# Performance work log

Measured on AMD Instinct MI355X. Metric: run time of the kernel, lower is better.

Reference implementation:

```python
import jax, jax.numpy as jnp
import numpy as np

D_K = 64
NEG_INF = -1.0e9

def setup_inputs() -> dict:
    key = jax.random.key(0)
    kq, kk, kv, km = jax.random.split(key, 4)
    B, H, S, D = 2, 16, 2048, D_K
    Q = jax.random.normal(kq, (B, H, S, D), dtype=jnp.float32)
    K = jax.random.normal(kk, (B, H, S, D), dtype=jnp.float32)
    V = jax.random.normal(kv, (B, H, S, D), dtype=jnp.float32)
    # True entries are masked out (torch masked_fill semantics)
    attn_mask = jax.random.randint(km, (B, H, S, S), 0, 2).astype(jnp.bool_)
    return {"Q": Q, "K": K, "V": V, "attn_mask": attn_mask}

def reference(Q, K, V, attn_mask):
    # scores: [B, H, len_q, len_k]
    scale = 1.0 / np.sqrt(D_K).astype(np.float32)
    scores = jnp.einsum('bhqd,bhkd->bhqk', Q, K) * scale
    scores = jnp.where(attn_mask, jnp.float32(NEG_INF), scores)
    attn = jax.nn.softmax(scores, axis=-1)
    prob = jnp.einsum('bhqk,bhkd->bhqd', attn, V)
    return (prob, attn)
```

## Files before the change

kernel.cpp:

```cpp
#include <hip/hip_runtime.h>
#include <hip/hip_bf16.h>

#define S_LEN 2048
#define D_DIM 64
#define QT    64
#define KT    64
#define NTHR  256
#define NKT   (S_LEN / KT)
#define NBLK  1024
#define PROB_ELEMS 4194304LL

typedef float        f32x4  __attribute__((ext_vector_type(4)));
typedef int          i32x4  __attribute__((ext_vector_type(4)));
typedef unsigned int u32x4  __attribute__((ext_vector_type(4)));
typedef short        bf16x8 __attribute__((ext_vector_type(8)));

__device__ __forceinline__ unsigned short f2bf(float f) {
    return __builtin_bit_cast(unsigned short, __float2bfloat16(f));
}
__device__ __forceinline__ int swzc(int row, int ch) {
    return ch ^ ((row ^ (row >> 3)) & 7);
}
__device__ __forceinline__ u32x4 packbf(float4 a, float4 b) {
    u32x4 r;
    r[0] = (unsigned)f2bf(a.x) | ((unsigned)f2bf(a.y) << 16);
    r[1] = (unsigned)f2bf(a.z) | ((unsigned)f2bf(a.w) << 16);
    r[2] = (unsigned)f2bf(b.x) | ((unsigned)f2bf(b.y) << 16);
    r[3] = (unsigned)f2bf(b.z) | ((unsigned)f2bf(b.w) << 16);
    return r;
}

__global__ void mask_probe_kernel(const unsigned int* __restrict__ m,
                                  int* __restrict__ flag) {
    unsigned int v = m[threadIdx.x];
    unsigned long long ok = __ballot(v <= 1u);
    if (threadIdx.x == 0) *flag = (ok == ~0ULL) ? 1 : 0;
}


#define LOAD_K(KP, KTV)                                                     \
    { _Pragma("unroll")                                                     \
      for (int i = 0; i < 2; ++i) {                                         \
        int flat = i * NTHR + t, row = flat >> 3, ch = flat & 7;            \
        const float* src = Kg + (kbase + (KTV) * KT + row) * D_DIM + ch * 8;\
        float4 a = *(const float4*)src, b = *(const float4*)(src + 4);      \
        KP[i] = packbf(a, b);                                               \
      } }

#define STAGE_K(KS, KP)                                                     \
    { _Pragma("unroll")                                                     \
      for (int i = 0; i < 2; ++i) {                                         \
        int flat = i * NTHR + t, row = flat >> 3, ch = flat & 7;            \
        *(u32x4*)((KS) + row * 128 + swzc(row, ch) * 16) = KP[i];           \
      } }

#define LOAD_V(VP, KTV)                                                     \
    { const float* src = Vg + (kbase + (KTV) * KT + k0v) * D_DIM + dgv * 8; \
      float4 a = *(const float4*)src, b = *(const float4*)(src + 4);        \
      float4 e4 = *(const float4*)(src + D_DIM);                            \
      float4 f4 = *(const float4*)(src + D_DIM + 4);                        \
      VP[0] = (unsigned)f2bf(a.x) | ((unsigned)f2bf(e4.x) << 16);           \
      VP[1] = (unsigned)f2bf(a.y) | ((unsigned)f2bf(e4.y) << 16);           \
      VP[2] = (unsigned)f2bf(a.z) | ((unsigned)f2bf(e4.z) << 16);           \
      VP[3] = (unsigned)f2bf(a.w) | ((unsigned)f2bf(e4.w) << 16);           \
      VP[4] = (unsigned)f2bf(b.x) | ((unsigned)f2bf(f4.x) << 16);           \
      VP[5] = (unsigned)f2bf(b.y) | ((unsigned)f2bf(f4.y) << 16);           \
      VP[6] = (unsigned)f2bf(b.z) | ((unsigned)f2bf(f4.z) << 16);           \
      VP[7] = (unsigned)f2bf(b.w) | ((unsigned)f2bf(f4.w) << 16); }

#define STAGE_V(VT, VP)                                                     \
    { _Pragma("unroll")                                                     \
      for (int jj = 0; jj < 8; ++jj) {                                      \
        int d = dgv * 8 + jj;                                               \
        *(unsigned*)((VT) + d * 128 + swzc(d, k0v >> 3) * 16 + (k0v & 7) * 2) = VP[jj]; \
      } }

#define LOAD_MBITS(DST, KTV)                                                \
    { unsigned bz = 0u;                                                     \
      _Pragma("unroll")                                                     \
      for (int n = 0; n < 4; ++n) {                                         \
        unsigned idx = rowoff + (unsigned)((KTV) * KT + n * 16 + 4 * g);    \
        if (mask32) {                                                       \
            i32x4 m4 = *(const i32x4*)(((const int*)maskB) + idx);          \
            bz |= ((m4[0] ? 1u : 0u) | (m4[1] ? 2u : 0u) |                  \
                   (m4[2] ? 4u : 0u) | (m4[3] ? 8u : 0u)) << (n * 4);       \
        } else {                                                            \
            unsigned mb = *(const unsigned*)(maskB + idx);                  \
            bz |= (((mb & 0xffu) ? 1u : 0u) | ((mb & 0xff00u) ? 2u : 0u) |  \
                   ((mb & 0xff0000u) ? 4u : 0u) |                           \
                   ((mb & 0xff000000u) ? 8u : 0u)) << (n * 4);              \
        } }                                                                 \
      (DST) = bz; }

#define LOAD_BITS2(DST, KTV)                                                \
    { if (useWS) (DST) = (unsigned)bitsWS[bitbase + (unsigned)(KTV) * NTHR];\
      else LOAD_MBITS(DST, KTV) }

#define PH1_TILE(KS, BITS)                                                  \
    { unsigned bb = (BITS);                                                 \
      _Pragma("unroll")                                                     \
      for (int n = 0; n < 4; ++n) {                                         \
        int rowk = n * 16 + c;                                              \
        bf16x8 kf0 = *(const bf16x8*)((KS) + rowk * 128 + swzc(rowk, g) * 16);     \
        bf16x8 kf1 = *(const bf16x8*)((KS) + rowk * 128 + swzc(rowk, 4 + g) * 16); \
        f32x4 acc = {0.f, 0.f, 0.f, 0.f};                                   \
        acc = __builtin_amdgcn_mfma_f32_16x16x32_bf16(kf0, qf0, acc, 0, 0, 0); \
        acc = __builtin_amdgcn_mfma_f32_16x16x32_bf16(kf1, qf1, acc, 0, 0, 0); \
        unsigned mb = bb >> (n * 4);                                        \
        psum += (mb & 1u) ? 0.f : __expf(acc[0] * 0.125f);                  \
        psum += (mb & 2u) ? 0.f : __expf(acc[1] * 0.125f);                  \
        psum += (mb & 4u) ? 0.f : __expf(acc[2] * 0.125f);                  \
        psum += (mb & 8u) ? 0.f : __expf(acc[3] * 0.125f);                  \
      } }

#define PH2_TILE(KS, VT, BITS, KTV)                                         \
    { unsigned bb = (BITS);                                                 \
      _Pragma("unroll")                                                     \
      for (int n = 0; n < 4; ++n) {                                         \
        int rowk = n * 16 + c;                                              \
        bf16x8 kf0 = *(const bf16x8*)((KS) + rowk * 128 + swzc(rowk, g) * 16);     \
        bf16x8 kf1 = *(const bf16x8*)((KS) + rowk * 128 + swzc(rowk, 4 + g) * 16); \
        f32x4 acc = {0.f, 0.f, 0.f, 0.f};                                   \
        acc = __builtin_amdgcn_mfma_f32_16x16x32_bf16(kf0, qf0, acc, 0, 0, 0); \
        acc = __builtin_amdgcn_mfma_f32_16x16x32_bf16(kf1, qf1, acc, 0, 0, 0); \
        unsigned mb = bb >> (n * 4);                                        \
        f32x4 ev;                                                           \
        ev[0] = (mb & 1u) ? 0.f : __expf(acc[0] * 0.125f) * rinv;           \
        ev[1] = (mb & 2u) ? 0.f : __expf(acc[1] * 0.125f) * rinv;           \
        ev[2] = (mb & 4u) ? 0.f : __expf(acc[2] * 0.125f) * rinv;           \
        ev[3] = (mb & 8u) ? 0.f : __expf(acc[3] * 0.125f) * rinv;           \
        unsigned idx0 = rowoff + (unsigned)((KTV) * KT + n * 16 + 4 * g);   \
        __builtin_nontemporal_store(ev, (f32x4*)(attnOut + idx0));          \
        unsigned p0 = (unsigned)f2bf(ev[0]) | ((unsigned)f2bf(ev[1]) << 16);\
        unsigned p1 = (unsigned)f2bf(ev[2]) | ((unsigned)f2bf(ev[3]) << 16);\
        int kloc = n * 16 + 4 * g;                                          \
        uint2 pkv; pkv.x = p0; pkv.y = p1;                                  \
        *(uint2*)(Ps + ql * 128 + swzc(ql, kloc >> 3) * 16 + (kloc & 7) * 2) = pkv; \
      }                                                                     \
             \
      { bf16x8 pa0 = *(const bf16x8*)(Ps + ql * 128 + swzc(ql, g) * 16);    \
        bf16x8 pa1 = *(const bf16x8*)(Ps + ql * 128 + swzc(ql, 4 + g) * 16);\
        _Pragma("unroll")                                                   \
        for (int df = 0; df < 4; ++df) {                                    \
            int d = df * 16 + c;                                            \
            bf16x8 vb0 = *(const bf16x8*)((VT) + d * 128 + swzc(d, g) * 16);     \
            bf16x8 vb1 = *(const bf16x8*)((VT) + d * 128 + swzc(d, 4 + g) * 16); \
            pacc[df] = __builtin_amdgcn_mfma_f32_16x16x32_bf16(pa0, vb0, pacc[df], 0, 0, 0); \
            pacc[df] = __builtin_amdgcn_mfma_f32_16x16x32_bf16(pa1, vb1, pacc[df], 0, 0, 0); \
        } } }

__global__ __launch_bounds__(NTHR, 4)
void attn_fused(const float* __restrict__ Qg, const float* __restrict__ Kg,
                const float* __restrict__ Vg,
                const unsigned char* __restrict__ maskB,
                const int* __restrict__ flagp,
                unsigned short* __restrict__ bitsWS, int useWS,
                float* __restrict__ attnOut, float* __restrict__ probOut) {
    __shared__ unsigned char sm[40960];
    unsigned char* Ks0 = sm;
    unsigned char* Ks1 = sm + 8192;
    unsigned char* Vt0 = sm + 16384;
    unsigned char* Vt1 = sm + 24576;
    unsigned char* Ps  = sm + 32768;

    const int t = threadIdx.x;
    const int lane = t & 63, w = t >> 6, c = lane & 15, g = lane >> 4;

    const int orig = blockIdx.x;
    const int virt = (orig & 7) * 128 + (orig >> 3);
    const int qt = virt & 31, bh = virt >> 5;
    const int mask32 = *flagp;

    const int qrowbase = bh * S_LEN + qt * QT;
    const int kbase = bh * S_LEN;
    const int ql = w * 16 + c;
    const unsigned rowoff = (unsigned)(qrowbase + ql) * (unsigned)S_LEN;
    const unsigned bitbase = (unsigned)virt * NKT * NTHR + (unsigned)t;
    const int dgv = t & 7, k0v = (t >> 3) * 2;

    #pragma unroll
    for (int i = 0; i < 2; ++i) {
        int flat = i * NTHR + t, row = flat >> 3, ch = flat & 7;
        const float* src = Qg + (qrowbase + row) * D_DIM + ch * 8;
        float4 a = *(const float4*)src, b = *(const float4*)(src + 4);
        *(u32x4*)(Ps + row * 128 + swzc(row, ch) * 16) = packbf(a, b);
    }
    __syncthreads();
    bf16x8 qf0 = *(const bf16x8*)(Ps + ql * 128 + swzc(ql, g) * 16);
    bf16x8 qf1 = *(const bf16x8*)(Ps + ql * 128 + swzc(ql, 4 + g) * 16);
    __syncthreads();

    float psum = 0.f;
    u32x4 kpA[2], kpB[2];
    unsigned bA, bB;

    LOAD_K(kpA, 0)
    LOAD_MBITS(bA, 0)

    for (int j = 0; j < NKT / 2; ++j) {
        const int ktA = 2 * j, ktB = 2 * j + 1;
        STAGE_K(Ks0, kpA)
        LOAD_K(kpB, ktB)
        LOAD_MBITS(bB, ktB)
        __syncthreads();
        PH1_TILE(Ks0, bA)
        if (useWS) bitsWS[bitbase + (unsigned)ktA * NTHR] = (unsigned short)bA;

        STAGE_K(Ks1, kpB)
        if (j + 1 < NKT / 2) {
            LOAD_K(kpA, ktA + 2)
            LOAD_MBITS(bA, ktA + 2)
        }
        __syncthreads();
        PH1_TILE(Ks1, bB)
        if (useWS) bitsWS[bitbase + (unsigned)ktB * NTHR] = (unsigned short)bB;
    }

    float s = psum;
    s += __shfl_xor(s, 16, 64);
    s += __shfl_xor(s, 32, 64);
    const float rinv = 1.0f / s;

    f32x4 pacc[4];
    #pragma unroll
    for (int d = 0; d < 4; ++d) pacc[d] = (f32x4){0.f, 0.f, 0.f, 0.f};

    unsigned vpA[8], vpB[8];
    LOAD_K(kpA, 0)
    LOAD_V(vpA, 0)
    LOAD_BITS2(bA, 0)
    __syncthreads();

    for (int j = 0; j < NKT / 2; ++j) {
        const int ktA = 2 * j, ktB = 2 * j + 1;
        STAGE_K(Ks0, kpA)
        STAGE_V(Vt0, vpA)
        LOAD_K(kpB, ktB)
        LOAD_V(vpB, ktB)
        LOAD_BITS2(bB, ktB)
        __syncthreads();
        PH2_TILE(Ks0, Vt0, bA, ktA)

        STAGE_K(Ks1, kpB)
        STAGE_V(Vt1, vpB)
        if (j + 1 < NKT / 2) {
            LOAD_K(kpA, ktA + 2)
            LOAD_V(vpA, ktA + 2)
            LOAD_BITS2(bA, ktA + 2)
        }
        __syncthreads();
        PH2_TILE(Ks1, Vt1, bB, ktB)
    }

    #pragma unroll
    for (int df = 0; df < 4; ++df)
        #pragma unroll
        for (int r = 0; r < 4; ++r) {
            int qe = w * 16 + g * 4 + r;
            probOut[(long long)(qrowbase + qe) * D_DIM + df * 16 + c] = pacc[df][r];
        }
}

extern "C" void kernel_launch(void* const* d_in, const int* in_sizes, int n_in,
                              void* d_out, int out_size, void* d_ws, size_t ws_size,
                              hipStream_t stream) {
    const float* Q = (const float*)d_in[0];
    const float* K = (const float*)d_in[1];
    const float* V = (const float*)d_in[2];
    const unsigned char* mask = (const unsigned char*)d_in[3];

    float* prob = (float*)d_out;
    float* attn = (float*)d_out + PROB_ELEMS;

    int* flag = (int*)d_ws;
    unsigned short* bitsWS = (unsigned short*)((char*)d_ws + 256);
    const size_t bits_bytes = (size_t)NBLK * NKT * NTHR * 2ull;
    const int useWS = (ws_size >= (size_t)256 + bits_bytes) ? 1 : 0;

    mask_probe_kernel<<<1, 64, 0, stream>>>((const unsigned int*)mask, flag);
    attn_fused<<<NBLK, NTHR, 0, stream>>>(Q, K, V, mask, flag, bitsWS, useWS,
                                          attn, prob);
}
```

Measured before the change: 412.6 us.

## Pre-convert K/V to swizzled bf16 tiles and stream them via global_load_lds

Adds a prep kernel that converts K and V once into pre-swizzled bf16 tiles, with V stored transposed, in workspace. The main kernel then loads those tiles straight into LDS with global_load_lds, so each of the 1024 blocks no longer repeats the fp32 load, convert and LDS store of K/V. Other changes fold the 1/sqrt(d) scale into Q, use v_cvt_pk_bf16_f32 for packing, and raise wave priority around the PV MFMAs. The cost is an extra launch and more workspace, with a register-path fallback when the workspace is too small.

```diff
diff --git a/kernel.cpp b/kernel.cpp
--- a/kernel.cpp
+++ b/kernel.cpp
@@ -21,6 +21,9 @@
 __device__ __forceinline__ int swzc(int row, int ch) {
     return ch ^ ((row ^ (row >> 3)) & 7);
 }
+__device__ __forceinline__ float4 scale4(float4 v, float s) {
+    v.x *= s; v.y *= s; v.z *= s; v.w *= s; return v;
+}
 __device__ __forceinline__ u32x4 packbf(float4 a, float4 b) {
     u32x4 r;
     r[0] = (unsigned)f2bf(a.x) | ((unsigned)f2bf(a.y) << 16);
@@ -29,6 +32,16 @@
     r[3] = (unsigned)f2bf(b.z) | ((unsigned)f2bf(b.w) << 16);
     return r;
 }
+__device__ __forceinline__ unsigned cvtpk(float lo, float hi) {
+    unsigned r;
+    asm("v_cvt_pk_bf16_f32 %0, %1, %2" : "=v"(r) : "v"(lo), "v"(hi));
+    return r;
+}
+__device__ __forceinline__ void glds16(const unsigned* g, unsigned char* l) {
+    __builtin_amdgcn_global_load_lds(
+        (const __attribute__((address_space(1))) unsigned*)g,
+        (__attribute__((address_space(3))) unsigned*)(void*)l, 16, 0, 0);
+}
 
 __global__ void mask_probe_kernel(const unsigned int* __restrict__ m,
                                   int* __restrict__ flag) {
@@ -37,43 +50,39 @@
     if (threadIdx.x == 0) *flag = (ok == ~0ULL) ? 1 : 0;
 }
 
-
-#define LOAD_K(KP, KTV)                                                     \
-    { _Pragma("unroll")                                                     \
-      for (int i = 0; i < 2; ++i) {                                         \
-        int flat = i * NTHR + t, row = flat >> 3, ch = flat & 7;            \
-        const float* src = Kg + (kbase + (KTV) * KT + row) * D_DIM + ch * 8;\
-        float4 a = *(const float4*)src, b = *(const float4*)(src + 4);      \
-        KP[i] = packbf(a, b);                                               \
-      } }
-
-#define STAGE_K(KS, KP)                                                     \
-    { _Pragma("unroll")                                                     \
-      for (int i = 0; i < 2; ++i) {                                         \
-        int flat = i * NTHR + t, row = flat >> 3, ch = flat & 7;            \
-        *(u32x4*)((KS) + row * 128 + swzc(row, ch) * 16) = KP[i];           \
-      } }
-
-#define LOAD_V(VP, KTV)                                                     \
-    { const float* src = Vg + (kbase + (KTV) * KT + k0v) * D_DIM + dgv * 8; \
-      float4 a = *(const float4*)src, b = *(const float4*)(src + 4);        \
-      float4 e4 = *(const float4*)(src + D_DIM);                            \
-      float4 f4 = *(const float4*)(src + D_DIM + 4);                        \
-      VP[0] = (unsigned)f2bf(a.x) | ((unsigned)f2bf(e4.x) << 16);           \
-      VP[1] = (unsigned)f2bf(a.y) | ((unsigned)f2bf(e4.y) << 16);           \
-      VP[2] = (unsigned)f2bf(a.z) | ((unsigned)f2bf(e4.z) << 16);           \
-      VP[3] = (unsigned)f2bf(a.w) | ((unsigned)f2bf(e4.w) << 16);           \
-      VP[4] = (unsigned)f2bf(b.x) | ((unsigned)f2bf(f4.x) << 16);           \
-      VP[5] = (unsigned)f2bf(b.y) | ((unsigned)f2bf(f4.y) << 16);           \
-      VP[6] = (unsigned)f2bf(b.z) | ((unsigned)f2bf(f4.z) << 16);           \
-      VP[7] = (unsigned)f2bf(b.w) | ((unsigned)f2bf(f4.w) << 16); }
-
-#define STAGE_V(VT, VP)                                                     \
-    { _Pragma("unroll")                                                     \
-      for (int jj = 0; jj < 8; ++jj) {                                      \
-        int d = dgv * 8 + jj;                                               \
-        *(unsigned*)((VT) + d * 128 + swzc(d, k0v >> 3) * 16 + (k0v & 7) * 2) = VP[jj]; \
-      } }
+#define KPART 524288
+#define VPART 65536
+__global__ __launch_bounds__(256)
+void kv_prep(const float* __restrict__ Kg, const float* __restrict__ Vg,
+             unsigned* __restrict__ Kbf, unsigned* __restrict__ Vtb) {
+    int tid = blockIdx.x * 256 + threadIdx.x;
+    if (tid < KPART) {
+        int ch = tid & 7, rowg = tid >> 3;
+        const float* src = Kg + (long long)rowg * D_DIM + ch * 8;
+        float4 a = *(const float4*)src, b = *(const float4*)(src + 4);
+        int bh = rowg >> 11, k = rowg & 2047, kt = k >> 6, row = k & 63;
+        unsigned* dst = Kbf + ((unsigned)(bh * NKT + kt) << 11)
+                            + row * 32 + swzc(row, ch) * 4;
+        *(u32x4*)dst = packbf(a, b);
+    } else if (tid < KPART + VPART) {
+        int idx = tid - KPART;
+        int d = idx & 63, kt = (idx >> 6) & 31, bh = idx >> 11;
+        const float* vb = Vg + (long long)(bh * S_LEN + kt * KT) * D_DIM + d;
+        unsigned* tile = Vtb + ((unsigned)(bh * NKT + kt) << 11) + d * 32;
+        #pragma unroll
+        for (int ci = 0; ci < 8; ++ci) {
+            u32x4 o;
+            #pragma unroll
+            for (int s = 0; s < 4; ++s) {
+                float lo = vb[(ci * 8 + 2 * s) * D_DIM];
+                float hi = vb[(ci * 8 + 2 * s + 1) * D_DIM];
+                o[s] = (unsigned)f2bf(lo) | ((unsigned)f2bf(hi) << 16);
+            }
+            *(u32x4*)(tile + swzc(d, ci) * 4) = o;
+        }
+    }
+}
+
 
 #define LOAD_MBITS(DST, KTV)                                                \
     { unsigned bz = 0u;                                                     \
@@ -107,10 +116,10 @@
         acc = __builtin_amdgcn_mfma_f32_16x16x32_bf16(kf0, qf0, acc, 0, 0, 0); \
         acc = __builtin_amdgcn_mfma_f32_16x16x32_bf16(kf1, qf1, acc, 0, 0, 0); \
         unsigned mb = bb >> (n * 4);                                        \
-        psum += (mb & 1u) ? 0.f : __expf(acc[0] * 0.125f);                  \
-        psum += (mb & 2u) ? 0.f : __expf(acc[1] * 0.125f);                  \
-        psum += (mb & 4u) ? 0.f : __expf(acc[2] * 0.125f);                  \
-        psum += (mb & 8u) ? 0.f : __expf(acc[3] * 0.125f);                  \
+        psum += (mb & 1u) ? 0.f : __expf(acc[0]);                           \
+        psum += (mb & 2u) ? 0.f : __expf(acc[1]);                           \
+        psum += (mb & 4u) ? 0.f : __expf(acc[2]);                           \
+        psum += (mb & 8u) ? 0.f : __expf(acc[3]);                           \
       } }
 
 #define PH2_TILE(KS, VT, BITS, KTV)                                         \
@@ -125,21 +134,19 @@
         acc = __builtin_amdgcn_mfma_f32_16x16x32_bf16(kf1, qf1, acc, 0, 0, 0); \
         unsigned mb = bb >> (n * 4);                                        \
         f32x4 ev;                                                           \
-        ev[0] = (mb & 1u) ? 0.f : __expf(acc[0] * 0.125f) * rinv;           \
-        ev[1] = (mb & 2u) ? 0.f : __expf(acc[1] * 0.125f) * rinv;           \
-        ev[2] = (mb & 4u) ? 0.f : __expf(acc[2] * 0.125f) * rinv;           \
-        ev[3] = (mb & 8u) ? 0.f : __expf(acc[3] * 0.125f) * rinv;           \
+        ev[0] = (mb & 1u) ? 0.f : __expf(acc[0]) * rinv;                    \
+        ev[1] = (mb & 2u) ? 0.f : __expf(acc[1]) * rinv;                    \
+        ev[2] = (mb & 4u) ? 0.f : __expf(acc[2]) * rinv;                    \
+        ev[3] = (mb & 8u) ? 0.f : __expf(acc[3]) * rinv;                    \
         unsigned idx0 = rowoff + (unsigned)((KTV) * KT + n * 16 + 4 * g);   \
         __builtin_nontemporal_store(ev, (f32x4*)(attnOut + idx0));          \
-        unsigned p0 = (unsigned)f2bf(ev[0]) | ((unsigned)f2bf(ev[1]) << 16);\
-        unsigned p1 = (unsigned)f2bf(ev[2]) | ((unsigned)f2bf(ev[3]) << 16);\
+        uint2 pkv; pkv.x = cvtpk(ev[0], ev[1]); pkv.y = cvtpk(ev[2], ev[3]);\
         int kloc = n * 16 + 4 * g;                                          \
-        uint2 pkv; pkv.x = p0; pkv.y = p1;                                  \
         *(uint2*)(Ps + ql * 128 + swzc(ql, kloc >> 3) * 16 + (kloc & 7) * 2) = pkv; \
       }                                                                     \
-             \
       { bf16x8 pa0 = *(const bf16x8*)(Ps + ql * 128 + swzc(ql, g) * 16);    \
         bf16x8 pa1 = *(const bf16x8*)(Ps + ql * 128 + swzc(ql, 4 + g) * 16);\
+        __builtin_amdgcn_s_setprio(1);                                      \
         _Pragma("unroll")                                                   \
         for (int df = 0; df < 4; ++df) {                                    \
             int d = df * 16 + c;                                            \
@@ -147,15 +154,17 @@
             bf16x8 vb1 = *(const bf16x8*)((VT) + d * 128 + swzc(d, 4 + g) * 16); \
             pacc[df] = __builtin_amdgcn_mfma_f32_16x16x32_bf16(pa0, vb0, pacc[df], 0, 0, 0); \
             pacc[df] = __builtin_amdgcn_mfma_f32_16x16x32_bf16(pa1, vb1, pacc[df], 0, 0, 0); \
-        } } }
+        }                                                                   \
+        __builtin_amdgcn_s_setprio(0); } }
 
 __global__ __launch_bounds__(NTHR, 4)
-void attn_fused(const float* __restrict__ Qg, const float* __restrict__ Kg,
-                const float* __restrict__ Vg,
-                const unsigned char* __restrict__ maskB,
-                const int* __restrict__ flagp,
-                unsigned short* __restrict__ bitsWS, int useWS,
-                float* __restrict__ attnOut, float* __restrict__ probOut) {
+void attn_fused_glds(const float* __restrict__ Qg,
+                     const unsigned* __restrict__ Kbf,
+                     const unsigned* __restrict__ Vtb,
+                     const unsigned char* __restrict__ maskB,
+                     const int* __restrict__ flagp,
+                     unsigned short* __restrict__ bitsWS, int useWS,
+                     float* __restrict__ attnOut, float* __restrict__ probOut) {
     __shared__ unsigned char sm[40960];
     unsigned char* Ks0 = sm;
     unsigned char* Ks1 = sm + 8192;
@@ -172,6 +181,164 @@
     const int mask32 = *flagp;
 
     const int qrowbase = bh * S_LEN + qt * QT;
+    const int ql = w * 16 + c;
+    const unsigned rowoff = (unsigned)(qrowbase + ql) * (unsigned)S_LEN;
+    const unsigned bitbase = (unsigned)virt * NKT * NTHR + (unsigned)t;
+    const unsigned ktile0 = (unsigned)(bh * NKT) << 11;
+
+    const int f0u = t * 4, f1u = (NTHR + t) * 4;
+    const int dst0 = (t & ~63) * 16, dst1 = (NTHR + (t & ~63)) * 16;
+
+    #pragma unroll
+    for (int i = 0; i < 2; ++i) {
+        int flat = i * NTHR + t, row = flat >> 3, ch = flat & 7;
+        const float* src = Qg + (qrowbase + row) * D_DIM + ch * 8;
+        float4 a = *(const float4*)src, b = *(const float4*)(src + 4);
+        *(u32x4*)(Ps + row * 128 + swzc(row, ch) * 16) =
+            packbf(scale4(a, 0.125f), scale4(b, 0.125f));
+    }
+    __syncthreads();
+    bf16x8 qf0 = *(const bf16x8*)(Ps + ql * 128 + swzc(ql, g) * 16);
+    bf16x8 qf1 = *(const bf16x8*)(Ps + ql * 128 + swzc(ql, 4 + g) * 16);
+
+    float psum = 0.f;
+    unsigned bA, bB;
+    {
+        const unsigned* kp = Kbf + ktile0;
+        glds16(kp + f0u, Ks0 + dst0);
+        glds16(kp + f1u, Ks0 + dst1);
+    }
+    LOAD_MBITS(bA, 0)
+
+    for (int j = 0; j < NKT / 2; ++j) {
+        const int ktA = 2 * j, ktB = 2 * j + 1;
+        __syncthreads();
+        {
+            const unsigned* kp = Kbf + ktile0 + (unsigned)ktB * 2048;
+            glds16(kp + f0u, Ks1 + dst0);
+            glds16(kp + f1u, Ks1 + dst1);
+        }
+        LOAD_MBITS(bB, ktB)
+        PH1_TILE(Ks0, bA)
+        if (useWS) bitsWS[bitbase + (unsigned)ktA * NTHR] = (unsigned short)bA;
+
+        __syncthreads();
+        if (j + 1 < NKT / 2) {
+            const unsigned* kp = Kbf + ktile0 + (unsigned)(ktA + 2) * 2048;
+            glds16(kp + f0u, Ks0 + dst0);
+            glds16(kp + f1u, Ks0 + dst1);
+            LOAD_MBITS(bA, ktA + 2)
+        }
+        PH1_TILE(Ks1, bB)
+        if (useWS) bitsWS[bitbase + (unsigned)ktB * NTHR] = (unsigned short)bB;
+    }
+
+    float s = psum;
+    s += __shfl_xor(s, 16, 64);
+    s += __shfl_xor(s, 32, 64);
+    const float rinv = 1.0f / s;
+
+    f32x4 pacc[4];
+    #pragma unroll
+    for (int d = 0; d < 4; ++d) pacc[d] = (f32x4){0.f, 0.f, 0.f, 0.f};
+
+    {
+        const unsigned* kp = Kbf + ktile0;
+        const unsigned* vp = Vtb + ktile0;
+        glds16(kp + f0u, Ks0 + dst0); glds16(kp + f1u, Ks0 + dst1);
+        glds16(vp + f0u, Vt0 + dst0); glds16(vp + f1u, Vt0 + dst1);
+    }
+    LOAD_BITS2(bA, 0)
+
+    for (int j = 0; j < NKT / 2; ++j) {
+        const int ktA = 2 * j, ktB = 2 * j + 1;
+        __syncthreads();
+        {
+            const unsigned* kp = Kbf + ktile0 + (unsigned)ktB * 2048;
+            const unsigned* vp = Vtb + ktile0 + (unsigned)ktB * 2048;
+            glds16(kp + f0u, Ks1 + dst0); glds16(kp + f1u, Ks1 + dst1);
+            glds16(vp + f0u, Vt1 + dst0); glds16(vp + f1u, Vt1 + dst1);
+        }
+        LOAD_BITS2(bB, ktB)
+        PH2_TILE(Ks0, Vt0, bA, ktA)
+
+        __syncthreads();
+        if (j + 1 < NKT / 2) {
+            const unsigned* kp = Kbf + ktile0 + (unsigned)(ktA + 2) * 2048;
+            const unsigned* vp = Vtb + ktile0 + (unsigned)(ktA + 2) * 2048;
+            glds16(kp + f0u, Ks0 + dst0); glds16(kp + f1u, Ks0 + dst1);
+            glds16(vp + f0u, Vt0 + dst0); glds16(vp + f1u, Vt0 + dst1);
+            LOAD_BITS2(bA, ktA + 2)
+        }
+        PH2_TILE(Ks1, Vt1, bB, ktB)
+    }
+
+    #pragma unroll
+    for (int df = 0; df < 4; ++df)
+        #pragma unroll
+        for (int r = 0; r < 4; ++r) {
+            int qe = w * 16 + g * 4 + r;
+            probOut[(long long)(qrowbase + qe) * D_DIM + df * 16 + c] = pacc[df][r];
+        }
+}
+
+#define LOAD_K(KP, KTV)                                                     \
+    { _Pragma("unroll")                                                     \
+      for (int i = 0; i < 2; ++i) {                                         \
+        int flat = i * NTHR + t, row = flat >> 3, ch = flat & 7;            \
+        const float* src = Kg + (kbase + (KTV) * KT + row) * D_DIM + ch * 8;\
+        float4 a = *(const float4*)src, b = *(const float4*)(src + 4);      \
+        KP[i] = packbf(a, b);                                               \
+      } }
+#define STAGE_K(KS, KP)                                                     \
+    { _Pragma("unroll")                                                     \
+      for (int i = 0; i < 2; ++i) {                                         \
+        int flat = i * NTHR + t, row = flat >> 3, ch = flat & 7;            \
+        *(u32x4*)((KS) + row * 128 + swzc(row, ch) * 16) = KP[i];           \
+      } }
+#define LOAD_V(VP, KTV)                                                     \
+    { const float* src = Vg + (kbase + (KTV) * KT + k0v) * D_DIM + dgv * 8; \
+      float4 a = *(const float4*)src, b = *(const float4*)(src + 4);        \
+      float4 e4 = *(const float4*)(src + D_DIM);                            \
+      float4 f4 = *(const float4*)(src + D_DIM + 4);                        \
+      VP[0] = (unsigned)f2bf(a.x) | ((unsigned)f2bf(e4.x) << 16);           \
+      VP[1] = (unsigned)f2bf(a.y) | ((unsigned)f2bf(e4.y) << 16);           \
+      VP[2] = (unsigned)f2bf(a.z) | ((unsigned)f2bf(e4.z) << 16);           \
+      VP[3] = (unsigned)f2bf(a.w) | ((unsigned)f2bf(e4.w) << 16);           \
+      VP[4] = (unsigned)f2bf(b.x) | ((unsigned)f2bf(f4.x) << 16);           \
+      VP[5] = (unsigned)f2bf(b.y) | ((unsigned)f2bf(f4.y) << 16);           \
+      VP[6] = (unsigned)f2bf(b.z) | ((unsigned)f2bf(f4.z) << 16);           \
+      VP[7] = (unsigned)f2bf(b.w) | ((unsigned)f2bf(f4.w) << 16); }
+#define STAGE_V(VT, VP)                                                     \
+    { _Pragma("unroll")                                                     \
+      for (int jj = 0; jj < 8; ++jj) {                                      \
+        int d = dgv * 8 + jj;                                               \
+        *(unsigned*)((VT) + d * 128 + swzc(d, k0v >> 3) * 16 + (k0v & 7) * 2) = VP[jj]; \
+      } }
+
+__global__ __launch_bounds__(NTHR, 4)
+void attn_fused_reg(const float* __restrict__ Qg, const float* __restrict__ Kg,
+                    const float* __restrict__ Vg,
+                    const unsigned char* __restrict__ maskB,
+                    const int* __restrict__ flagp,
+                    unsigned short* __restrict__ bitsWS, int useWS,
+                    float* __restrict__ attnOut, float* __restrict__ probOut) {
+    __shared__ unsigned char sm[40960];
+    unsigned char* Ks0 = sm;
+    unsigned char* Ks1 = sm + 8192;
+    unsigned char* Vt0 = sm + 16384;
+    unsigned char* Vt1 = sm + 24576;
+    unsigned char* Ps  = sm + 32768;
+
+    const int t = threadIdx.x;
+    const int lane = t & 63, w = t >> 6, c = lane & 15, g = lane >> 4;
+
+    const int orig = blockIdx.x;
+    const int virt = (orig & 7) * 128 + (orig >> 3);
+    const int qt = virt & 31, bh = virt >> 5;
+    const int mask32 = *flagp;
+
+    const int qrowbase = bh * S_LEN + qt * QT;
     const int kbase = bh * S_LEN;
     const int ql = w * 16 + c;
     const unsigned rowoff = (unsigned)(qrowbase + ql) * (unsigned)S_LEN;
@@ -183,7 +350,8 @@
         int flat = i * NTHR + t, row = flat >> 3, ch = flat & 7;
         const float* src = Qg + (qrowbase + row) * D_DIM + ch * 8;
         float4 a = *(const float4*)src, b = *(const float4*)(src + 4);
-        *(u32x4*)(Ps + row * 128 + swzc(row, ch) * 16) = packbf(a, b);
+        *(u32x4*)(Ps + row * 128 + swzc(row, ch) * 16) =
+            packbf(scale4(a, 0.125f), scale4(b, 0.125f));
     }
     __syncthreads();
     bf16x8 qf0 = *(const bf16x8*)(Ps + ql * 128 + swzc(ql, g) * 16);
@@ -193,7 +361,6 @@
     float psum = 0.f;
     u32x4 kpA[2], kpB[2];
     unsigned bA, bB;
-
     LOAD_K(kpA, 0)
     LOAD_MBITS(bA, 0)
 
@@ -205,7 +372,6 @@
         __syncthreads();
         PH1_TILE(Ks0, bA)
         if (useWS) bitsWS[bitbase + (unsigned)ktA * NTHR] = (unsigned short)bA;
-
         STAGE_K(Ks1, kpB)
         if (j + 1 < NKT / 2) {
             LOAD_K(kpA, ktA + 2)
@@ -240,7 +406,6 @@
         LOAD_BITS2(bB, ktB)
         __syncthreads();
         PH2_TILE(Ks0, Vt0, bA, ktA)
-
         STAGE_K(Ks1, kpB)
         STAGE_V(Vt1, vpB)
         if (j + 1 < NKT / 2) {
@@ -272,12 +437,23 @@
     float* prob = (float*)d_out;
     float* attn = (float*)d_out + PROB_ELEMS;
 
+    const size_t bits_bytes = (size_t)NBLK * NKT * NTHR * 2ull;
+    const size_t kbf_bytes  = 8388608ull;
     int* flag = (int*)d_ws;
     unsigned short* bitsWS = (unsigned short*)((char*)d_ws + 256);
-    const size_t bits_bytes = (size_t)NBLK * NKT * NTHR * 2ull;
-    const int useWS = (ws_size >= (size_t)256 + bits_bytes) ? 1 : 0;
+    unsigned* Kbf = (unsigned*)((char*)d_ws + 256 + bits_bytes);
+    unsigned* Vtb = (unsigned*)((char*)d_ws + 256 + bits_bytes + kbf_bytes);
+
+    const int useWS   = (ws_size >= 256 + bits_bytes) ? 1 : 0;
+    const int usePrep = (ws_size >= 256 + bits_bytes + 2 * kbf_bytes) ? 1 : 0;
 
     mask_probe_kernel<<<1, 64, 0, stream>>>((const unsigned int*)mask, flag);
-    attn_fused<<<NBLK, NTHR, 0, stream>>>(Q, K, V, mask, flag, bitsWS, useWS,
-                                          attn, prob);
-}
+    if (usePrep) {
+        kv_prep<<<(KPART + VPART) / 256, 256, 0, stream>>>(K, V, Kbf, Vtb);
+        attn_fused_glds<<<NBLK, NTHR, 0, stream>>>(Q, Kbf, Vtb, mask, flag,
+                                                   bitsWS, useWS, attn, prob);
+    } else {
+        attn_fused_reg<<<NBLK, NTHR, 0, stream>>>(Q, K, V, mask, flag,
+                                                  bitsWS, useWS, attn, prob);
+    }
+}
```

Measured after the change: 365.3 us, median of 3. 11.5% less time.
